# Kernel optimization log

Measured on AMD Instinct MI355X. Metric: run time of the kernel, lower is better.

The kernel has to match this reference:

```python
import jax, jax.numpy as jnp
import numpy as np

H = 1024      # hidden_size
L = 4         # num_layers
DI = 2 * H    # d_inner (expand=2)
N = 16        # d_state
K = 4         # d_conv
BATCH = 2
S = 1024
EPS = 1e-5


def _layernorm(x, g, b):
    mu = jnp.mean(x, axis=-1, keepdims=True)
    xc = x - mu
    var = jnp.mean(xc * xc, axis=-1, keepdims=True)
    return xc * jax.lax.rsqrt(var + EPS) * g + b


def _causal_dwconv(x, w, b):
    # x: [B,S,DI], w: [DI,K], b: [DI]. Torch Conv1d(pad=K-1, groups=DI) truncated to S == causal left-pad conv.
    xp = jnp.pad(x, ((0, 0), (K - 1, 0), (0, 0)))
    s = x.shape[1]
    y = sum(xp[:, k:k + s, :] * w[:, k] for k in range(K))
    return y + b


def _forward(hidden_states, in_norm_g, in_norm_b, ln_g, ln_b, in_proj_w,
             conv_w, conv_b, x_proj_w, dt_proj_w, dt_proj_b, D,
             mamba_ln_g, mamba_ln_b, out_proj_w, op1_w, op1_b, op2_w, op2_b):
    dtype = hidden_states.dtype
    A = -jnp.arange(1, N + 1, dtype=dtype)  # [N]; == -exp(log(arange)), identical across d_inner rows
    x = _layernorm(hidden_states, in_norm_g, in_norm_b)
    for l in range(L):
        res_x = x
        xn = _layernorm(x, ln_g[l], ln_b[l])
        xr = jnp.einsum('bsh,ph->bsp', xn, in_proj_w[l])           # [B,S,2*DI]
        x_inner, res = jnp.split(xr, 2, axis=-1)
        x_inner = jax.nn.silu(x_inner)
        for c in range(2):
            x_inner = jax.nn.silu(_causal_dwconv(x_inner, conv_w[l, c], conv_b[l, c]))
        proj = jnp.einsum('bsd,pd->bsp', x_inner, x_proj_w[l])     # [B,S,1+2N]
        dt_raw, Bm, Cm = proj[..., :1], proj[..., 1:1 + N], proj[..., 1 + N:]
        dt = jax.nn.softplus(dt_raw * dt_proj_w[l][:, 0] + dt_proj_b[l])  # [B,S,DI]

        def step(h, inp_t):
            dt_t, x_t, B_t, C_t = inp_t                      # [B,DI],[B,DI],[B,N],[B,N]
            h = h + dt_t[..., None] * (h * A + x_t[..., None] * B_t[:, None, :])
            y = jnp.einsum('bdn,bn->bd', h, C_t)
            return h, y

        h0 = jnp.zeros((x.shape[0], DI, N), dtype=dtype)
        xs = (dt.transpose(1, 0, 2), x_inner.transpose(1, 0, 2),
              Bm.transpose(1, 0, 2), Cm.transpose(1, 0, 2))
        _, ys = jax.lax.scan(step, h0, xs)                   # ys: [S,B,DI]
        y = ys.transpose(1, 0, 2)
        y = y + x_inner * D[l]
        y = _layernorm(y, mamba_ln_g[l], mamba_ln_b[l])
        y = y * jax.nn.sigmoid(res)
        x = res_x + jnp.einsum('bsd,hd->bsh', y, out_proj_w[l])
    out = jax.nn.gelu(x @ op1_w.T + op1_b, approximate=False) @ op2_w.T + op2_b
    return out + hidden_states


def setup_inputs() -> dict:
    key = jax.random.key(0)
    ks = jax.random.split(key, 10)
    rn = lambda k, shape, s: jax.random.normal(k, shape, dtype=jnp.float32) * s
    return {
        'hidden_states': rn(ks[0], (BATCH, S, H), 1.0),
        'in_norm_g': jnp.ones((H,), jnp.float32),
        'in_norm_b': jnp.zeros((H,), jnp.float32),
        'ln_g': jnp.ones((L, H), jnp.float32),
        'ln_b': jnp.zeros((L, H), jnp.float32),
        'in_proj_w': rn(ks[1], (L, 2 * DI, H), 0.02),
        'conv_w': rn(ks[2], (L, 2, DI, K), 0.2),
        'conv_b': jnp.zeros((L, 2, DI), jnp.float32),
        'x_proj_w': rn(ks[3], (L, 1 + 2 * N, DI), 0.02),
        'dt_proj_w': rn(ks[4], (L, DI, 1), 0.01),
        'dt_proj_b': jnp.full((L, DI), -4.0, jnp.float32),  # keeps dt small -> stable scan
        'D': jnp.ones((L, DI), jnp.float32),
        'mamba_ln_g': jnp.ones((L, DI), jnp.float32),
        'mamba_ln_b': jnp.zeros((L, DI), jnp.float32),
        'out_proj_w': rn(ks[5], (L, H, DI), 0.02),
        'op1_w': rn(ks[6], (H, H), 0.02),
        'op1_b': jnp.zeros((H,), jnp.float32),
        'op2_w': rn(ks[7], (H, H), 0.02),
        'op2_b': jnp.zeros((H,), jnp.float32),
    }


def reference(hidden_states, in_norm_g, in_norm_b, ln_g, ln_b, in_proj_w,
              conv_w, conv_b, x_proj_w, dt_proj_w, dt_proj_b, D,
              mamba_ln_g, mamba_ln_b, out_proj_w, op1_w, op1_b, op2_w, op2_b):
    return _forward(hidden_states, in_norm_g, in_norm_b, ln_g, ln_b, in_proj_w,
                    conv_w, conv_b, x_proj_w, dt_proj_w, dt_proj_b, D,
                    mamba_ln_g, mamba_ln_b, out_proj_w, op1_w, op1_b, op2_w, op2_b)
```

## Files before the change

### kernel.cpp

```cpp
#include <hip/hip_runtime.h>
#include <hip/hip_bf16.h>
#include <math.h>

constexpr int HDIM = 1024;
constexpr int LNUM = 4;
constexpr int DINNER = 2048;
constexpr int KCONV = 4;
constexpr int NB = 2;
constexpr int SLEN = 1024;
constexpr int TOK = NB * SLEN;
constexpr float LNEPS = 1e-5f;

constexpr int NCHUNK = 32;
constexpr int CLEN = SLEN / NCHUNK;
constexpr int PROW = 36;
constexpr int XPN = 48;
constexpr int XSPLIT = 8;
constexpr int CCH = 32;

typedef __attribute__((ext_vector_type(8))) short short8;
typedef __attribute__((ext_vector_type(4))) float f32x4;

__device__ __forceinline__ __hip_bfloat16 f2bf(float x) { return __float2bfloat16(x); }
__device__ __forceinline__ unsigned short f2bfu(float x) {
    __hip_bfloat16 h = __float2bfloat16(x);
    return *(unsigned short*)&h;
}
__device__ __forceinline__ float sigmoidf_(float x) { return 1.f / (1.f + __expf(-x)); }
__device__ __forceinline__ float siluf_(float x) { return x / (1.f + __expf(-x)); }
__device__ __forceinline__ float softplusf_(float x) { return (x > 20.f) ? x : log1pf(__expf(x)); }

__device__ __forceinline__ void cp16(const void* g, void* l) {
    __builtin_amdgcn_global_load_lds(
        (const __attribute__((address_space(1))) unsigned int*)g,
        (__attribute__((address_space(3))) unsigned int*)l, 16, 0, 0);
}

__global__ __launch_bounds__(256) void cvt_k(const float* __restrict__ in,
                                             __hip_bfloat16* __restrict__ out, int n4)
{
    const int i = blockIdx.x * 256 + threadIdx.x;
    if (i >= n4) return;
    float4 v = ((const float4*)in)[i];
    ushort4 o;
    o.x = f2bfu(v.x); o.y = f2bfu(v.y); o.z = f2bfu(v.z); o.w = f2bfu(v.w);
    ((ushort4*)out)[i] = o;
}

__global__ __launch_bounds__(256) void cvtwx_k(const float* __restrict__ in,
                                               __hip_bfloat16* __restrict__ out)
{
    const int i = blockIdx.x * 256 + threadIdx.x;
    if (i >= LNUM * XPN * DINNER / 4) return;
    const int e = i * 4;
    const int l = e / (XPN * DINNER);
    const int rem = e - l * XPN * DINNER;
    const int r = rem >> 11;
    const int col = rem & (DINNER - 1);
    ushort4 o;
    if (r < 33) {
        float4 v = *(const float4*)&in[(((size_t)l * 33 + r) << 11) + col];
        o.x = f2bfu(v.x); o.y = f2bfu(v.y); o.z = f2bfu(v.z); o.w = f2bfu(v.w);
    } else {
        o.x = o.y = o.z = o.w = 0;
    }
    ((ushort4*)out)[i] = o;
}

template<int MODE, int D>
__global__ __launch_bounds__(256) void ln_k(
    const float* __restrict__ in, const float* __restrict__ g, const float* __restrict__ b,
    float* __restrict__ outF, __hip_bfloat16* __restrict__ outB,
    const float* __restrict__ gate, int gstride)
{
    constexpr int EPT = D / 1024;
    const int t = blockIdx.x, tid = threadIdx.x;
    float4 v[EPT];
    float s1 = 0.f, s2 = 0.f;
#pragma unroll
    for (int i = 0; i < EPT; ++i) {
        const int idx = (tid + i * 256) * 4;
        float4 val = *(const float4*)&in[(size_t)t * D + idx];
        v[i] = val;
        s1 += val.x + val.y + val.z + val.w;
        s2 += val.x * val.x + val.y * val.y + val.z * val.z + val.w * val.w;
    }
#pragma unroll
    for (int off = 32; off; off >>= 1) { s1 += __shfl_down(s1, off); s2 += __shfl_down(s2, off); }
    __shared__ float rs[4], rq[4];
    const int w = tid >> 6, lane = tid & 63;
    if (lane == 0) { rs[w] = s1; rq[w] = s2; }
    __syncthreads();
    const float mu = (rs[0] + rs[1] + rs[2] + rs[3]) * (1.f / D);
    const float ms = (rq[0] + rq[1] + rq[2] + rq[3]) * (1.f / D);
    const float var = ms - mu * mu;
    const float rstd = rsqrtf((var > 0.f ? var : 0.f) + LNEPS);
#pragma unroll
    for (int i = 0; i < EPT; ++i) {
        const int idx = (tid + i * 256) * 4;
        const float4 gg = *(const float4*)&g[idx];
        const float4 bb = *(const float4*)&b[idx];
        float4 o;
        o.x = (v[i].x - mu) * rstd * gg.x + bb.x;
        o.y = (v[i].y - mu) * rstd * gg.y + bb.y;
        o.z = (v[i].z - mu) * rstd * gg.z + bb.z;
        o.w = (v[i].w - mu) * rstd * gg.w + bb.w;
        if (MODE == 2) {
            const float4 gt = *(const float4*)&gate[(size_t)t * gstride + idx];
            o.x *= sigmoidf_(gt.x); o.y *= sigmoidf_(gt.y);
            o.z *= sigmoidf_(gt.z); o.w *= sigmoidf_(gt.w);
        }
        if (MODE == 0) {
            ((float4*)outF)[((size_t)t * D + idx) >> 2] = o;
        } else {
            ushort4 u;
            u.x = f2bfu(o.x); u.y = f2bfu(o.y); u.z = f2bfu(o.z); u.w = f2bfu(o.w);
            ((ushort4*)outB)[((size_t)t * D + idx) >> 2] = u;
        }
    }
}

__global__ __launch_bounds__(256) void xcomb_ln_k(
    const float* __restrict__ part, float* __restrict__ x,
    const float* __restrict__ g, const float* __restrict__ b,
    __hip_bfloat16* __restrict__ outB)
{
    const int t = blockIdx.x, tid = threadIdx.x;
    const int idx = tid * 4;
    const size_t off = (size_t)t * HDIM + idx;
    float4 a = *(const float4*)&part[off];
    float4 c = *(const float4*)&part[(size_t)TOK * HDIM + off];
    float4 v = *(const float4*)&x[off];
    v.x += a.x + c.x; v.y += a.y + c.y; v.z += a.z + c.z; v.w += a.w + c.w;
    *(float4*)&x[off] = v;
    float s1 = v.x + v.y + v.z + v.w;
    float s2 = v.x * v.x + v.y * v.y + v.z * v.z + v.w * v.w;
#pragma unroll
    for (int o2 = 32; o2; o2 >>= 1) { s1 += __shfl_down(s1, o2); s2 += __shfl_down(s2, o2); }
    __shared__ float rs[4], rq[4];
    const int w = tid >> 6, lane = tid & 63;
    if (lane == 0) { rs[w] = s1; rq[w] = s2; }
    __syncthreads();
    const float mu = (rs[0] + rs[1] + rs[2] + rs[3]) * (1.f / HDIM);
    const float ms = (rq[0] + rq[1] + rq[2] + rq[3]) * (1.f / HDIM);
    const float var = ms - mu * mu;
    const float rstd = rsqrtf((var > 0.f ? var : 0.f) + LNEPS);
    const float4 gg = *(const float4*)&g[idx];
    const float4 bb = *(const float4*)&b[idx];
    ushort4 u;
    u.x = f2bfu((v.x - mu) * rstd * gg.x + bb.x);
    u.y = f2bfu((v.y - mu) * rstd * gg.y + bb.y);
    u.z = f2bfu((v.z - mu) * rstd * gg.z + bb.z);
    u.w = f2bfu((v.w - mu) * rstd * gg.w + bb.w);
    ((ushort4*)outB)[off >> 2] = u;
}

__global__ __launch_bounds__(256) void xcomb_cast_k(
    const float* __restrict__ part, const float* __restrict__ x,
    __hip_bfloat16* __restrict__ xn, int n4)
{
    const int i = blockIdx.x * 256 + threadIdx.x;
    if (i >= n4) return;
    float4 a = ((const float4*)part)[i];
    float4 c = ((const float4*)part)[i + n4];
    float4 v = ((const float4*)x)[i];
    v.x += a.x + c.x; v.y += a.y + c.y; v.z += a.z + c.z; v.w += a.w + c.w;
    ushort4 u;
    u.x = f2bfu(v.x); u.y = f2bfu(v.y); u.z = f2bfu(v.z); u.w = f2bfu(v.w);
    ((ushort4*)xn)[i] = u;
}

template<int EPI>
__global__ __launch_bounds__(256) void gemm_bt(
    const unsigned short* __restrict__ A, const unsigned short* __restrict__ B,
    int M, int N, int Kd,
    float* __restrict__ Cf, __hip_bfloat16* __restrict__ Cb,
    const float* __restrict__ bias, const float* __restrict__ res,
    float* __restrict__ Of)
{
    __shared__ __align__(16) unsigned short As[2][128 * 32];
    __shared__ __align__(16) unsigned short Bs[2][128 * 32];
    const int tid = threadIdx.x;
    const int m0 = blockIdx.x * 128, n0 = blockIdx.y * 128;
    const int klen = Kd / (int)gridDim.z;
    const int kstart = (int)blockIdx.z * klen;
    const int nK = klen >> 5;
    const int wave = tid >> 6, lane = tid & 63;
    const int wm = (wave & 1) * 64, wn = (wave >> 1) * 64;
    const int quad = lane >> 4, l16 = lane & 15;
    f32x4 acc[4][4];
#pragma unroll
    for (int i = 0; i < 4; ++i)
#pragma unroll
        for (int j = 0; j < 4; ++j) acc[i][j] = (f32x4){0.f, 0.f, 0.f, 0.f};

    const int r1 = tid >> 2, kc1 = (tid & 3) * 8;
    const int r2 = r1 + 64;

    {
        const int k0 = kstart;
        cp16(&A[(size_t)(m0 + r1) * Kd + k0 + kc1], &As[0][tid * 8]);
        cp16(&A[(size_t)(m0 + r2) * Kd + k0 + kc1], &As[0][(tid + 256) * 8]);
        cp16(&B[(size_t)(n0 + r1) * Kd + k0 + kc1], &Bs[0][tid * 8]);
        cp16(&B[(size_t)(n0 + r2) * Kd + k0 + kc1], &Bs[0][(tid + 256) * 8]);
    }
    for (int kk = 0; kk < nK; ++kk) {
        __syncthreads();
        if (kk + 1 < nK) {
            const int k0 = kstart + ((kk + 1) << 5);
            const int nb = (kk + 1) & 1;
            cp16(&A[(size_t)(m0 + r1) * Kd + k0 + kc1], &As[nb][tid * 8]);
            cp16(&A[(size_t)(m0 + r2) * Kd + k0 + kc1], &As[nb][(tid + 256) * 8]);
            cp16(&B[(size_t)(n0 + r1) * Kd + k0 + kc1], &Bs[nb][tid * 8]);
            cp16(&B[(size_t)(n0 + r2) * Kd + k0 + kc1], &Bs[nb][(tid + 256) * 8]);
        }
        const int cb = kk & 1;
        short8 af[4], bfm[4];
#pragma unroll
        for (int i = 0; i < 4; ++i) af[i]  = *(const short8*)&As[cb][(wm + i * 16 + l16) * 32 + quad * 8];
#pragma unroll
        for (int j = 0; j < 4; ++j) bfm[j] = *(const short8*)&Bs[cb][(wn + j * 16 + l16) * 32 + quad * 8];
#pragma unroll
        for (int i = 0; i < 4; ++i)
#pragma unroll
            for (int j = 0; j < 4; ++j)
                acc[i][j] = __builtin_amdgcn_mfma_f32_16x16x32_bf16(af[i], bfm[j], acc[i][j], 0, 0, 0);
    }

    const size_t zoff = (EPI == 1) ? (size_t)blockIdx.z * M * N : 0;
#pragma unroll
    for (int i = 0; i < 4; ++i)
#pragma unroll
        for (int j = 0; j < 4; ++j)
#pragma unroll
            for (int r = 0; r < 4; ++r) {
                const int row = m0 + wm + i * 16 + quad * 4 + r;
                const int col = n0 + wn + j * 16 + l16;
                const size_t off = (size_t)row * N + col;
                float vv = acc[i][j][r];
                if (EPI == 0) {
                    Cf[off] = vv;
                } else if (EPI == 1) {
                    Cf[zoff + off] = vv;
                } else if (EPI == 2) {
                    float z = vv + bias[col];
                    Cb[off] = f2bf(0.5f * z * (1.f + erff(z * 0.70710678118f)));
                } else {
                    Of[off] = vv + bias[col] + res[off];
                }
            }
}

__global__ __launch_bounds__(256) void pcomb_k(const float* __restrict__ ppart,
                                               float* __restrict__ proj)
{
    const int idx = blockIdx.x * 256 + threadIdx.x;
    if (idx >= TOK * 33) return;
    const int t = idx / 33, p2 = idx - t * 33;
    float s = 0.f;
#pragma unroll
    for (int k = 0; k < XSPLIT; ++k)
        s += ppart[(size_t)k * TOK * XPN + (size_t)t * XPN + p2];
    proj[idx] = s;
}

__global__ __launch_bounds__(256) void conv2_fused(
    const float* __restrict__ xin, int in_stride,
    const float* __restrict__ cw, const float* __restrict__ cb, int layer,
    float* __restrict__ out, __hip_bfloat16* __restrict__ outb)
{
    const int d = blockIdx.x * 256 + threadIdx.x;
    const int s0 = blockIdx.y * CCH;
    const int b = blockIdx.z;
    float w1k[4], w2k[4];
#pragma unroll
    for (int k = 0; k < 4; ++k) {
        w1k[k] = cw[(((size_t)layer * 2 + 0) * DINNER + d) * KCONV + k];
        w2k[k] = cw[(((size_t)layer * 2 + 1) * DINNER + d) * KCONV + k];
    }
    const float b1 = cb[((size_t)layer * 2 + 0) * DINNER + d];
    const float b2 = cb[((size_t)layer * 2 + 1) * DINNER + d];
    const float* base = xin + (size_t)b * SLEN * in_stride + d;

    float xv[CCH + 6];
#pragma unroll
    for (int i = 0; i < CCH + 6; ++i) {
        const int s = s0 - 6 + i;
        const int sc = (s < 0) ? 0 : s;
        xv[i] = base[(size_t)sc * in_stride];
    }
#pragma unroll
    for (int i = 0; i < CCH + 6; ++i) {
        const int s = s0 - 6 + i;
        xv[i] = (s >= 0) ? siluf_(xv[i]) : 0.f;
    }
    float c1[CCH + 3];
#pragma unroll
    for (int i = 0; i < CCH + 3; ++i) {
        const int s = s0 - 3 + i;
        float t = fmaf(w1k[0], xv[i], fmaf(w1k[1], xv[i + 1],
                  fmaf(w1k[2], xv[i + 2], fmaf(w1k[3], xv[i + 3], b1))));
        c1[i] = (s >= 0) ? siluf_(t) : 0.f;
    }
    const size_t obase = (size_t)b * SLEN * DINNER + d;
#pragma unroll
    for (int j = 0; j < CCH; ++j) {
        float t2 = fmaf(w2k[0], c1[j], fmaf(w2k[1], c1[j + 1],
                   fmaf(w2k[2], c1[j + 2], fmaf(w2k[3], c1[j + 3], b2))));
        const float v = siluf_(t2);
        out[obase + (size_t)(s0 + j) * DINNER] = v;
        outb[obase + (size_t)(s0 + j) * DINNER] = f2bf(v);
    }
}

__global__ __launch_bounds__(256) void xproj_mfma(
    const unsigned short* __restrict__ A, const unsigned short* __restrict__ B,
    float* __restrict__ ppart)
{
    __shared__ __align__(16) unsigned short As[2][128 * 32];
    __shared__ __align__(16) unsigned short Bs[2][XPN * 32];
    const int tid = threadIdx.x;
    const int m0 = blockIdx.x * 128;
    const int k0base = blockIdx.y * (DINNER / XSPLIT);
    constexpr int nK = (DINNER / XSPLIT) >> 5;
    const int wave = tid >> 6, lane = tid & 63;
    const int wm = wave * 32;
    const int quad = lane >> 4, l16 = lane & 15;
    f32x4 acc[2][3];
#pragma unroll
    for (int i = 0; i < 2; ++i)
#pragma unroll
        for (int j = 0; j < 3; ++j) acc[i][j] = (f32x4){0.f, 0.f, 0.f, 0.f};

    const int r1 = tid >> 2, kc1 = (tid & 3) * 8;
    {
        const int k0 = k0base;
        cp16(&A[(size_t)(m0 + r1) * DINNER + k0 + kc1], &As[0][tid * 8]);
        cp16(&A[(size_t)(m0 + r1 + 64) * DINNER + k0 + kc1], &As[0][(tid + 256) * 8]);
        if (tid < XPN * 4)
            cp16(&B[(size_t)r1 * DINNER + k0 + kc1], &Bs[0][tid * 8]);
    }
    for (int kk = 0; kk < nK; ++kk) {
        __syncthreads();
        if (kk + 1 < nK) {
            const int k0 = k0base + ((kk + 1) << 5);
            const int nb = (kk + 1) & 1;
            cp16(&A[(size_t)(m0 + r1) * DINNER + k0 + kc1], &As[nb][tid * 8]);
            cp16(&A[(size_t)(m0 + r1 + 64) * DINNER + k0 + kc1], &As[nb][(tid + 256) * 8]);
            if (tid < XPN * 4)
                cp16(&B[(size_t)r1 * DINNER + k0 + kc1], &Bs[nb][tid * 8]);
        }
        const int cb = kk & 1;
        short8 af[2], bfm[3];
#pragma unroll
        for (int i = 0; i < 2; ++i) af[i]  = *(const short8*)&As[cb][(wm + i * 16 + l16) * 32 + quad * 8];
#pragma unroll
        for (int j = 0; j < 3; ++j) bfm[j] = *(const short8*)&Bs[cb][(j * 16 + l16) * 32 + quad * 8];
#pragma unroll
        for (int i = 0; i < 2; ++i)
#pragma unroll
            for (int j = 0; j < 3; ++j)
                acc[i][j] = __builtin_amdgcn_mfma_f32_16x16x32_bf16(af[i], bfm[j], acc[i][j], 0, 0, 0);
    }
    float* pp = ppart + (size_t)blockIdx.y * TOK * XPN;
#pragma unroll
    for (int i = 0; i < 2; ++i)
#pragma unroll
        for (int j = 0; j < 3; ++j) {
            const int col = j * 16 + l16;
#pragma unroll
            for (int r = 0; r < 4; ++r) {
                const int row = m0 + wm + i * 16 + quad * 4 + r;
                pp[(size_t)row * XPN + col] = acc[i][j][r];
            }
        }
}

__device__ __forceinline__ void load_proj_chunk(float* sp, const float* __restrict__ proj,
                                                int b, int c, int tid)
{
    const float* psrc = proj + ((size_t)b * SLEN + (size_t)c * CLEN) * 33;
    for (int i = tid; i < CLEN * 33; i += 256) {
        int s = i / 33, p = i - s * 33;
        sp[s * PROW + (p == 0 ? 32 : p - 1)] = psrc[i];
    }
}

__global__ __launch_bounds__(256) void scan_partA(
    const float* __restrict__ proj, const float* __restrict__ xin,
    const float* __restrict__ dtw, const float* __restrict__ dtb, int layer,
    float* __restrict__ hloc, float* __restrict__ cumA_g)
{
    __shared__ __align__(16) float sp[CLEN * PROW];
    const int tid = threadIdx.x;
    const int d = blockIdx.x * 256 + tid;
    const int c = blockIdx.y, b = blockIdx.z;
    load_proj_chunk(sp, proj, b, c, tid);
    const float w_ = dtw[(size_t)layer * DINNER + d];
    const float bb = dtb[(size_t)layer * DINNER + d];
    __syncthreads();
    float h[16], ca[16];
#pragma unroll
    for (int n = 0; n < 16; ++n) { h[n] = 0.f; ca[n] = 1.f; }
    const float* xrow = xin + ((size_t)b * SLEN + (size_t)c * CLEN) * DINNER + d;
    float xt_next = xrow[0];
    for (int s = 0; s < CLEN; ++s) {
        const float xt = xt_next;
        if (s + 1 < CLEN) xt_next = xrow[(size_t)(s + 1) * DINNER];
        const float* row = &sp[s * PROW];
        const float dt = softplusf_(fmaf(row[32], w_, bb));
        const float u = dt * xt;
#pragma unroll
        for (int n = 0; n < 16; ++n) {
            const float a = fmaf(dt, -(float)(n + 1), 1.f);
            h[n] = fmaf(h[n], a, u * row[n]);
            ca[n] *= a;
        }
    }
    const size_t base = (((size_t)b * NCHUNK + c) * 16) * DINNER + d;
#pragma unroll
    for (int n = 0; n < 16; ++n) {
        hloc[base + (size_t)n * DINNER] = h[n];
        cumA_g[base + (size_t)n * DINNER] = ca[n];
    }
}

__global__ __launch_bounds__(256) void scan_combine(
    const float* __restrict__ hloc, const float* __restrict__ cumA_g,
    float* __restrict__ hin)
{
    const int idx = blockIdx.x * 256 + threadIdx.x;
    const int d = idx & (DINNER - 1);
    const int n = (idx >> 11) & 15;
    const int b = idx >> 15;
    float h = 0.f;
    for (int c = 0; c < NCHUNK; ++c) {
        const size_t off = (((size_t)b * NCHUNK + c) * 16 + n) * DINNER + d;
        hin[off] = h;
        h = fmaf(cumA_g[off], h, hloc[off]);
    }
}

__global__ __launch_bounds__(256) void scan_partC(
    const float* __restrict__ proj, const float* __restrict__ xin,
    const float* __restrict__ dtw, const float* __restrict__ dtb,
    const float* __restrict__ Dp, int layer,
    const float* __restrict__ hin, float* __restrict__ y)
{
    __shared__ __align__(16) float sp[CLEN * PROW];
    const int tid = threadIdx.x;
    const int d = blockIdx.x * 256 + tid;
    const int c = blockIdx.y, b = blockIdx.z;
    load_proj_chunk(sp, proj, b, c, tid);
    const float w_ = dtw[(size_t)layer * DINNER + d];
    const float bb = dtb[(size_t)layer * DINNER + d];
    const float Dd = Dp[(size_t)layer * DINNER + d];
    __syncthreads();
    float h[16];
    const size_t base = (((size_t)b * NCHUNK + c) * 16) * DINNER + d;
#pragma unroll
    for (int n = 0; n < 16; ++n) h[n] = hin[base + (size_t)n * DINNER];
    const float* xrow = xin + ((size_t)b * SLEN + (size_t)c * CLEN) * DINNER + d;
    float* yrow = y + ((size_t)b * SLEN + (size_t)c * CLEN) * DINNER + d;
    float xt_next = xrow[0];
    for (int s = 0; s < CLEN; ++s) {
        const float xt = xt_next;
        if (s + 1 < CLEN) xt_next = xrow[(size_t)(s + 1) * DINNER];
        const float* row = &sp[s * PROW];
        const float dt = softplusf_(fmaf(row[32], w_, bb));
        const float u = dt * xt;
        float yp = 0.f;
#pragma unroll
        for (int n = 0; n < 16; ++n) {
            const float a = fmaf(dt, -(float)(n + 1), 1.f);
            h[n] = fmaf(h[n], a, u * row[n]);
            yp = fmaf(h[n], row[16 + n], yp);
        }
        yrow[(size_t)s * DINNER] = yp + xt * Dd;
    }
}

extern "C" void kernel_launch(void* const* d_in, const int* in_sizes, int n_in,
                              void* d_out, int out_size, void* d_ws, size_t ws_size,
                              hipStream_t stream)
{
    (void)in_sizes; (void)n_in; (void)out_size;
    const float* hs   = (const float*)d_in[0];
    const float* ing  = (const float*)d_in[1];
    const float* inb  = (const float*)d_in[2];
    const float* lng  = (const float*)d_in[3];
    const float* lnb  = (const float*)d_in[4];
    const float* ipw  = (const float*)d_in[5];
    const float* cw   = (const float*)d_in[6];
    const float* cbp  = (const float*)d_in[7];
    const float* xpw  = (const float*)d_in[8];
    const float* dtw  = (const float*)d_in[9];
    const float* dtb  = (const float*)d_in[10];
    const float* Dp   = (const float*)d_in[11];
    const float* mlg  = (const float*)d_in[12];
    const float* mlb  = (const float*)d_in[13];
    const float* opw  = (const float*)d_in[14];
    const float* w1f  = (const float*)d_in[15];
    const float* b1f  = (const float*)d_in[16];
    const float* w2f  = (const float*)d_in[17];
    const float* b2f  = (const float*)d_in[18];

    char* p = (char*)d_ws;
    float* x   = (float*)p; p += (size_t)TOK * HDIM * 4;
    float* xr  = (float*)p; p += (size_t)TOK * 2 * DINNER * 4;
    float* c2  = (float*)p; p += (size_t)TOK * DINNER * 4;
    float* yb  = (float*)p; p += (size_t)TOK * DINNER * 4;
    float* proj= (float*)p; p += ((size_t)TOK * 33 * 4 + 255) & ~(size_t)255;
    float* hin = (float*)p; p += (size_t)NB * NCHUNK * 16 * DINNER * 4;
    float* ppart=(float*)p; p += (size_t)XSPLIT * TOK * XPN * 4;
    __hip_bfloat16* xn  = (__hip_bfloat16*)p; p += (size_t)TOK * HDIM * 2;
    __hip_bfloat16* y2  = (__hip_bfloat16*)p; p += (size_t)TOK * DINNER * 2;
    __hip_bfloat16* c2b = (__hip_bfloat16*)p; p += (size_t)TOK * DINNER * 2;
    __hip_bfloat16* wx  = (__hip_bfloat16*)p; p += (size_t)LNUM * XPN * DINNER * 2;
    __hip_bfloat16* t1 = (__hip_bfloat16*)xr;
    float* hloc = yb;
    float* cumA = yb + (size_t)NB * NCHUNK * 16 * DINNER;
    float* opart = c2;

    const size_t IPL = (size_t)2 * DINNER * HDIM;
    const size_t OPL = (size_t)HDIM * DINNER;
    const size_t MLPW = (size_t)HDIM * HDIM;

    size_t used = (size_t)(p - (char*)d_ws);
    const bool bulk = (used + (IPL * LNUM + OPL * LNUM + 2 * MLPW) * 2) <= ws_size;

    __hip_bfloat16 *wi[LNUM], *wo[LNUM], *w1, *w2;
    if (bulk) {
        for (int l = 0; l < LNUM; ++l) { wi[l] = (__hip_bfloat16*)p; p += IPL * 2; }
        for (int l = 0; l < LNUM; ++l) { wo[l] = (__hip_bfloat16*)p; p += OPL * 2; }
        w1 = (__hip_bfloat16*)p; p += MLPW * 2;
        w2 = (__hip_bfloat16*)p; p += MLPW * 2;
    } else {
        __hip_bfloat16* slotA = (__hip_bfloat16*)p; p += IPL * 2;
        __hip_bfloat16* slotB = (__hip_bfloat16*)p; p += OPL * 2;
        for (int l = 0; l < LNUM; ++l) { wi[l] = slotA; wo[l] = slotB; }
        w1 = slotA; w2 = slotB;
    }

    cvtwx_k<<<(LNUM * XPN * DINNER / 4 + 255) / 256, 256, 0, stream>>>(xpw, wx);

    if (bulk) {
        cvt_k<<<(int)(IPL * LNUM / 4 / 256), 256, 0, stream>>>(ipw, wi[0], (int)(IPL * LNUM / 4));
        cvt_k<<<(int)(OPL * LNUM / 4 / 256), 256, 0, stream>>>(opw, wo[0], (int)(OPL * LNUM / 4));
        cvt_k<<<(int)(MLPW / 4 / 256), 256, 0, stream>>>(w1f, w1, (int)(MLPW / 4));
        cvt_k<<<(int)(MLPW / 4 / 256), 256, 0, stream>>>(w2f, w2, (int)(MLPW / 4));
    }

    ln_k<0, HDIM><<<TOK, 256, 0, stream>>>(hs, ing, inb, x, nullptr, nullptr, 0);
    ln_k<1, HDIM><<<TOK, 256, 0, stream>>>(x, lng, lnb, nullptr, xn, nullptr, 0);

    for (int l = 0; l < LNUM; ++l) {
        if (!bulk)
            cvt_k<<<(int)(IPL / 4 / 256), 256, 0, stream>>>(ipw + (size_t)l * IPL, wi[l], (int)(IPL / 4));
        gemm_bt<0><<<dim3(TOK / 128, (2 * DINNER) / 128), 256, 0, stream>>>(
            (const unsigned short*)xn, (const unsigned short*)wi[l],
            TOK, 2 * DINNER, HDIM, xr, nullptr, nullptr, nullptr, nullptr);

        conv2_fused<<<dim3(DINNER / 256, SLEN / CCH, NB), 256, 0, stream>>>(
            xr, 2 * DINNER, cw, cbp, l, c2, c2b);

        xproj_mfma<<<dim3(TOK / 128, XSPLIT), 256, 0, stream>>>(
            (const unsigned short*)c2b, (const unsigned short*)(wx + (size_t)l * XPN * DINNER), ppart);
        pcomb_k<<<(TOK * 33 + 255) / 256, 256, 0, stream>>>(ppart, proj);

        scan_partA<<<dim3(DINNER / 256, NCHUNK, NB), 256, 0, stream>>>(
            proj, c2, dtw, dtb, l, hloc, cumA);
        scan_combine<<<(NB * 16 * DINNER) / 256, 256, 0, stream>>>(hloc, cumA, hin);
        scan_partC<<<dim3(DINNER / 256, NCHUNK, NB), 256, 0, stream>>>(
            proj, c2, dtw, dtb, Dp, l, hin, yb);

        ln_k<2, DINNER><<<TOK, 256, 0, stream>>>(yb, mlg + (size_t)l * DINNER, mlb + (size_t)l * DINNER,
                                                 nullptr, y2, xr + DINNER, 2 * DINNER);

        if (!bulk)
            cvt_k<<<(int)(OPL / 4 / 256), 256, 0, stream>>>(opw + (size_t)l * OPL, wo[l], (int)(OPL / 4));
        gemm_bt<1><<<dim3(TOK / 128, HDIM / 128, 2), 256, 0, stream>>>(
            (const unsigned short*)y2, (const unsigned short*)wo[l],
            TOK, HDIM, DINNER, opart, nullptr, nullptr, nullptr, nullptr);
        if (l + 1 < LNUM) {
            xcomb_ln_k<<<TOK, 256, 0, stream>>>(opart, x,
                lng + (size_t)(l + 1) * HDIM, lnb + (size_t)(l + 1) * HDIM, xn);
        } else {
            xcomb_cast_k<<<(TOK * HDIM / 4 + 255) / 256, 256, 0, stream>>>(
                opart, x, xn, TOK * HDIM / 4);
        }
    }

    if (!bulk) {
        cvt_k<<<(int)(MLPW / 4 / 256), 256, 0, stream>>>(w1f, w1, (int)(MLPW / 4));
        cvt_k<<<(int)(MLPW / 4 / 256), 256, 0, stream>>>(w2f, w2, (int)(MLPW / 4));
    }
    gemm_bt<2><<<dim3(TOK / 128, HDIM / 128), 256, 0, stream>>>(
        (const unsigned short*)xn, (const unsigned short*)w1,
        TOK, HDIM, HDIM, nullptr, t1, b1f, nullptr, nullptr);
    gemm_bt<3><<<dim3(TOK / 128, HDIM / 128), 256, 0, stream>>>(
        (const unsigned short*)t1, (const unsigned short*)w2,
        TOK, HDIM, HDIM, nullptr, nullptr, b2f, hs, (float*)d_out);
}
```

Measured before the change: 864.0 us.

## Split scan state dimension across two blocks and sum partial outputs in norm

The chunked selective scan kernels now split the 16 state channels into two halves handled by separate blocks, doubling the grid from 512 to 1024 blocks and halving per-thread register state. scan_partC writes two partial y buffers, one carrying the D skip term, and a new ynorm_k sums them before the gated layernorm. The aim is more parallelism and occupancy in the latency-bound scan, at the cost of an extra full-size fp32 y buffer write and read, plus duplicated x loads and softplus work per half.

```diff
diff --git a/kernel.cpp b/kernel.cpp
--- a/kernel.cpp
+++ b/kernel.cpp
@@ -70,8 +70,7 @@
 template<int MODE, int D>
 __global__ __launch_bounds__(256) void ln_k(
     const float* __restrict__ in, const float* __restrict__ g, const float* __restrict__ b,
-    float* __restrict__ outF, __hip_bfloat16* __restrict__ outB,
-    const float* __restrict__ gate, int gstride)
+    float* __restrict__ outF, __hip_bfloat16* __restrict__ outB)
 {
     constexpr int EPT = D / 1024;
     const int t = blockIdx.x, tid = threadIdx.x;
@@ -105,11 +104,6 @@
         o.y = (v[i].y - mu) * rstd * gg.y + bb.y;
         o.z = (v[i].z - mu) * rstd * gg.z + bb.z;
         o.w = (v[i].w - mu) * rstd * gg.w + bb.w;
-        if (MODE == 2) {
-            const float4 gt = *(const float4*)&gate[(size_t)t * gstride + idx];
-            o.x *= sigmoidf_(gt.x); o.y *= sigmoidf_(gt.y);
-            o.z *= sigmoidf_(gt.z); o.w *= sigmoidf_(gt.w);
-        }
         if (MODE == 0) {
             ((float4*)outF)[((size_t)t * D + idx) >> 2] = o;
         } else {
@@ -117,6 +111,53 @@
             u.x = f2bfu(o.x); u.y = f2bfu(o.y); u.z = f2bfu(o.z); u.w = f2bfu(o.w);
             ((ushort4*)outB)[((size_t)t * D + idx) >> 2] = u;
         }
+    }
+}
+
+__global__ __launch_bounds__(256) void ynorm_k(
+    const float* __restrict__ inA, const float* __restrict__ inB,
+    const float* __restrict__ g, const float* __restrict__ b,
+    __hip_bfloat16* __restrict__ outB,
+    const float* __restrict__ gate, int gstride)
+{
+    constexpr int D = DINNER;
+    constexpr int EPT = D / 1024;
+    const int t = blockIdx.x, tid = threadIdx.x;
+    float4 v[EPT];
+    float s1 = 0.f, s2 = 0.f;
+#pragma unroll
+    for (int i = 0; i < EPT; ++i) {
+        const int idx = (tid + i * 256) * 4;
+        float4 a = *(const float4*)&inA[(size_t)t * D + idx];
+        float4 c = *(const float4*)&inB[(size_t)t * D + idx];
+        float4 val;
+        val.x = a.x + c.x; val.y = a.y + c.y; val.z = a.z + c.z; val.w = a.w + c.w;
+        v[i] = val;
+        s1 += val.x + val.y + val.z + val.w;
+        s2 += val.x * val.x + val.y * val.y + val.z * val.z + val.w * val.w;
+    }
+#pragma unroll
+    for (int off = 32; off; off >>= 1) { s1 += __shfl_down(s1, off); s2 += __shfl_down(s2, off); }
+    __shared__ float rs[4], rq[4];
+    const int w = tid >> 6, lane = tid & 63;
+    if (lane == 0) { rs[w] = s1; rq[w] = s2; }
+    __syncthreads();
+    const float mu = (rs[0] + rs[1] + rs[2] + rs[3]) * (1.f / D);
+    const float ms = (rq[0] + rq[1] + rq[2] + rq[3]) * (1.f / D);
+    const float var = ms - mu * mu;
+    const float rstd = rsqrtf((var > 0.f ? var : 0.f) + LNEPS);
+#pragma unroll
+    for (int i = 0; i < EPT; ++i) {
+        const int idx = (tid + i * 256) * 4;
+        const float4 gg = *(const float4*)&g[idx];
+        const float4 bb = *(const float4*)&b[idx];
+        const float4 gt = *(const float4*)&gate[(size_t)t * gstride + idx];
+        ushort4 u;
+        u.x = f2bfu(((v[i].x - mu) * rstd * gg.x + bb.x) * sigmoidf_(gt.x));
+        u.y = f2bfu(((v[i].y - mu) * rstd * gg.y + bb.y) * sigmoidf_(gt.y));
+        u.z = f2bfu(((v[i].z - mu) * rstd * gg.z + bb.z) * sigmoidf_(gt.z));
+        u.w = f2bfu(((v[i].w - mu) * rstd * gg.w + bb.w) * sigmoidf_(gt.w));
+        ((ushort4*)outB)[((size_t)t * D + idx) >> 2] = u;
     }
 }
 
@@ -393,35 +434,37 @@
 {
     __shared__ __align__(16) float sp[CLEN * PROW];
     const int tid = threadIdx.x;
-    const int d = blockIdx.x * 256 + tid;
+    const int ns = blockIdx.x & 1;
+    const int d = (blockIdx.x >> 1) * 256 + tid;
     const int c = blockIdx.y, b = blockIdx.z;
     load_proj_chunk(sp, proj, b, c, tid);
     const float w_ = dtw[(size_t)layer * DINNER + d];
     const float bb = dtb[(size_t)layer * DINNER + d];
+    const float n0f = (float)(ns * 8);
     __syncthreads();
-    float h[16], ca[16];
-#pragma unroll
-    for (int n = 0; n < 16; ++n) { h[n] = 0.f; ca[n] = 1.f; }
+    float h[8], ca[8];
+#pragma unroll
+    for (int j = 0; j < 8; ++j) { h[j] = 0.f; ca[j] = 1.f; }
     const float* xrow = xin + ((size_t)b * SLEN + (size_t)c * CLEN) * DINNER + d;
     float xt_next = xrow[0];
     for (int s = 0; s < CLEN; ++s) {
         const float xt = xt_next;
         if (s + 1 < CLEN) xt_next = xrow[(size_t)(s + 1) * DINNER];
-        const float* row = &sp[s * PROW];
-        const float dt = softplusf_(fmaf(row[32], w_, bb));
+        const float* row = &sp[s * PROW] + ns * 8;
+        const float dt = softplusf_(fmaf(sp[s * PROW + 32], w_, bb));
         const float u = dt * xt;
 #pragma unroll
-        for (int n = 0; n < 16; ++n) {
-            const float a = fmaf(dt, -(float)(n + 1), 1.f);
-            h[n] = fmaf(h[n], a, u * row[n]);
-            ca[n] *= a;
+        for (int j = 0; j < 8; ++j) {
+            const float a = fmaf(dt, -(n0f + (float)(j + 1)), 1.f);
+            h[j] = fmaf(h[j], a, u * row[j]);
+            ca[j] *= a;
         }
     }
-    const size_t base = (((size_t)b * NCHUNK + c) * 16) * DINNER + d;
-#pragma unroll
-    for (int n = 0; n < 16; ++n) {
-        hloc[base + (size_t)n * DINNER] = h[n];
-        cumA_g[base + (size_t)n * DINNER] = ca[n];
+    const size_t base = (((size_t)b * NCHUNK + c) * 16 + ns * 8) * DINNER + d;
+#pragma unroll
+    for (int j = 0; j < 8; ++j) {
+        hloc[base + (size_t)j * DINNER] = h[j];
+        cumA_g[base + (size_t)j * DINNER] = ca[j];
     }
 }
 
@@ -445,38 +488,40 @@
     const float* __restrict__ proj, const float* __restrict__ xin,
     const float* __restrict__ dtw, const float* __restrict__ dtb,
     const float* __restrict__ Dp, int layer,
-    const float* __restrict__ hin, float* __restrict__ y)
+    const float* __restrict__ hin, float* __restrict__ yA, float* __restrict__ yB)
 {
     __shared__ __align__(16) float sp[CLEN * PROW];
     const int tid = threadIdx.x;
-    const int d = blockIdx.x * 256 + tid;
+    const int ns = blockIdx.x & 1;
+    const int d = (blockIdx.x >> 1) * 256 + tid;
     const int c = blockIdx.y, b = blockIdx.z;
     load_proj_chunk(sp, proj, b, c, tid);
     const float w_ = dtw[(size_t)layer * DINNER + d];
     const float bb = dtb[(size_t)layer * DINNER + d];
-    const float Dd = Dp[(size_t)layer * DINNER + d];
+    const float dmul = ns ? 0.f : Dp[(size_t)layer * DINNER + d];
+    const float n0f = (float)(ns * 8);
     __syncthreads();
-    float h[16];
-    const size_t base = (((size_t)b * NCHUNK + c) * 16) * DINNER + d;
-#pragma unroll
-    for (int n = 0; n < 16; ++n) h[n] = hin[base + (size_t)n * DINNER];
+    float h[8];
+    const size_t base = (((size_t)b * NCHUNK + c) * 16 + ns * 8) * DINNER + d;
+#pragma unroll
+    for (int j = 0; j < 8; ++j) h[j] = hin[base + (size_t)j * DINNER];
     const float* xrow = xin + ((size_t)b * SLEN + (size_t)c * CLEN) * DINNER + d;
-    float* yrow = y + ((size_t)b * SLEN + (size_t)c * CLEN) * DINNER + d;
+    float* yrow = (ns ? yB : yA) + ((size_t)b * SLEN + (size_t)c * CLEN) * DINNER + d;
     float xt_next = xrow[0];
     for (int s = 0; s < CLEN; ++s) {
         const float xt = xt_next;
         if (s + 1 < CLEN) xt_next = xrow[(size_t)(s + 1) * DINNER];
-        const float* row = &sp[s * PROW];
-        const float dt = softplusf_(fmaf(row[32], w_, bb));
+        const float* row = &sp[s * PROW] + ns * 8;
+        const float dt = softplusf_(fmaf(sp[s * PROW + 32], w_, bb));
         const float u = dt * xt;
         float yp = 0.f;
 #pragma unroll
-        for (int n = 0; n < 16; ++n) {
-            const float a = fmaf(dt, -(float)(n + 1), 1.f);
-            h[n] = fmaf(h[n], a, u * row[n]);
-            yp = fmaf(h[n], row[16 + n], yp);
+        for (int j = 0; j < 8; ++j) {
+            const float a = fmaf(dt, -(n0f + (float)(j + 1)), 1.f);
+            h[j] = fmaf(h[j], a, u * row[j]);
+            yp = fmaf(h[j], row[16 + j], yp);
         }
-        yrow[(size_t)s * DINNER] = yp + xt * Dd;
+        yrow[(size_t)s * DINNER] = yp + xt * dmul;
     }
 }
 
@@ -510,6 +555,7 @@
     float* xr  = (float*)p; p += (size_t)TOK * 2 * DINNER * 4;
     float* c2  = (float*)p; p += (size_t)TOK * DINNER * 4;
     float* yb  = (float*)p; p += (size_t)TOK * DINNER * 4;
+    float* yb2 = (float*)p; p += (size_t)TOK * DINNER * 4;
     float* proj= (float*)p; p += ((size_t)TOK * 33 * 4 + 255) & ~(size_t)255;
     float* hin = (float*)p; p += (size_t)NB * NCHUNK * 16 * DINNER * 4;
     float* ppart=(float*)p; p += (size_t)XSPLIT * TOK * XPN * 4;
@@ -551,8 +597,8 @@
         cvt_k<<<(int)(MLPW / 4 / 256), 256, 0, stream>>>(w2f, w2, (int)(MLPW / 4));
     }
 
-    ln_k<0, HDIM><<<TOK, 256, 0, stream>>>(hs, ing, inb, x, nullptr, nullptr, 0);
-    ln_k<1, HDIM><<<TOK, 256, 0, stream>>>(x, lng, lnb, nullptr, xn, nullptr, 0);
+    ln_k<0, HDIM><<<TOK, 256, 0, stream>>>(hs, ing, inb, x, nullptr);
+    ln_k<1, HDIM><<<TOK, 256, 0, stream>>>(x, lng, lnb, nullptr, xn);
 
     for (int l = 0; l < LNUM; ++l) {
         if (!bulk)
@@ -568,14 +614,14 @@
             (const unsigned short*)c2b, (const unsigned short*)(wx + (size_t)l * XPN * DINNER), ppart);
         pcomb_k<<<(TOK * 33 + 255) / 256, 256, 0, stream>>>(ppart, proj);
 
-        scan_partA<<<dim3(DINNER / 256, NCHUNK, NB), 256, 0, stream>>>(
+        scan_partA<<<dim3(DINNER / 256 * 2, NCHUNK, NB), 256, 0, stream>>>(
             proj, c2, dtw, dtb, l, hloc, cumA);
         scan_combine<<<(NB * 16 * DINNER) / 256, 256, 0, stream>>>(hloc, cumA, hin);
-        scan_partC<<<dim3(DINNER / 256, NCHUNK, NB), 256, 0, stream>>>(
-            proj, c2, dtw, dtb, Dp, l, hin, yb);
-
-        ln_k<2, DINNER><<<TOK, 256, 0, stream>>>(yb, mlg + (size_t)l * DINNER, mlb + (size_t)l * DINNER,
-                                                 nullptr, y2, xr + DINNER, 2 * DINNER);
+        scan_partC<<<dim3(DINNER / 256 * 2, NCHUNK, NB), 256, 0, stream>>>(
+            proj, c2, dtw, dtb, Dp, l, hin, yb, yb2);
+
+        ynorm_k<<<TOK, 256, 0, stream>>>(yb, yb2, mlg + (size_t)l * DINNER, mlb + (size_t)l * DINNER,
+                                         y2, xr + DINNER, 2 * DINNER);
 
         if (!bulk)
             cvt_k<<<(int)(OPL / 4 / 256), 256, 0, stream>>>(opw + (size_t)l * OPL, wo[l], (int)(OPL / 4));
```

New measurement: 950.6 us. 10.0% more time.
